# Optimization experiments

Measured on AMD Instinct MI355X. Metric: run time of the kernel, lower is better.

## Reference

```python
import jax, jax.numpy as jnp
import numpy as np

# ---- static LSS config (matches init_kwargs) ----
B, N = 4, 6
OGFH, OGFW, DS = 256, 704, 16
FH, FW = OGFH // DS, OGFW // DS            # 16, 44
D_LO, D_HI, D_STEP = 4.0, 45.0, 1.0
D = 41                                      # len(arange(4,45,1))
CAMC = 64
NX, NY, NZ = 200, 200, 1
DX = np.array([0.5, 0.5, 20.0], np.float32)
BX = np.array([-50.0 + 0.25, -50.0 + 0.25, -10.0 + 10.0], np.float32)  # lower + dx/2


def make_frustum():
    ds = jnp.arange(D_LO, D_HI, D_STEP, dtype=jnp.float32)[:, None, None]  # (D,1,1)
    xs = jnp.linspace(0.0, OGFW - 1.0, FW, dtype=jnp.float32)[None, None, :]
    ys = jnp.linspace(0.0, OGFH - 1.0, FH, dtype=jnp.float32)[None, :, None]
    ds, ys, xs = jnp.broadcast_arrays(ds, ys, xs)
    return jnp.stack([xs, ys, ds], axis=-1)  # (D, FH, FW, 3)


def setup_inputs() -> dict:
    key = jax.random.key(0)
    k1, k2 = jax.random.split(key)
    # depthnet output (pre-softmax depth logits + context features)
    x_feats = jax.random.normal(k1, (B, N, D + CAMC, FH, FW), dtype=jnp.float32)
    # cam-to-ego rotation: camera z (depth) -> ego x, so points land in the grid
    R = np.array([[0.0, 0.0, 1.0], [-1.0, 0.0, 0.0], [0.0, -1.0, 0.0]], np.float32)
    rots = jnp.asarray(np.broadcast_to(R, (B, N, 3, 3)).copy())
    trans = jax.random.normal(k2, (B, N, 3), dtype=jnp.float32) * 0.5
    f, cx, cy = 500.0, OGFW / 2.0, OGFH / 2.0
    K = np.array([[f, 0.0, cx], [0.0, f, cy], [0.0, 0.0, 1.0]], np.float32)
    intrins = jnp.asarray(np.broadcast_to(K, (B, N, 3, 3)).copy())
    post_rots = jnp.asarray(np.broadcast_to(np.eye(3, dtype=np.float32), (B, N, 3, 3)).copy())
    post_trans = jnp.zeros((B, N, 3), dtype=jnp.float32)
    return {"x_feats": x_feats, "rots": rots, "trans": trans,
            "intrins": intrins, "post_rots": post_rots, "post_trans": post_trans}


def reference(x_feats, rots, trans, intrins, post_rots, post_trans):
    # ---- lift: depth distribution x context features ----
    depth = jax.nn.softmax(x_feats[:, :, :D], axis=2)           # (B,N,D,h,w)
    feat = x_feats[:, :, D:D + CAMC]                            # (B,N,C,h,w)
    lifted = jnp.einsum('bndhw,bnchw->bndhwc', depth, feat)     # (B,N,D,h,w,C)

    # ---- geometry: per-pixel 3D points in ego frame ----
    frustum = make_frustum()                                    # (D,h,w,3)
    pts = frustum[None, None] - post_trans[:, :, None, None, None, :]
    pts = jnp.einsum('bnij,bndhwj->bndhwi', jnp.linalg.inv(post_rots), pts)
    pts = jnp.concatenate([pts[..., :2] * pts[..., 2:3], pts[..., 2:3]], axis=-1)
    combine = rots @ jnp.linalg.inv(intrins)
    pts = jnp.einsum('bnij,bndhwj->bndhwi', combine, pts) + trans[:, :, None, None, None, :]

    # ---- voxel pooling (scatter-add == bev_pool sum) ----
    dx = jnp.asarray(DX); bx = jnp.asarray(BX)
    gidx = jnp.floor((pts - (bx - dx / 2.0)) / dx).astype(jnp.int32)  # (B,N,D,h,w,3)
    ix, iy, iz = gidx[..., 0], gidx[..., 1], gidx[..., 2]
    valid = (ix >= 0) & (ix < NX) & (iy >= 0) & (iy < NY) & (iz >= 0) & (iz < NZ)
    b_ix = jnp.arange(B, dtype=jnp.int32)[:, None, None, None, None]
    flat = ((b_ix * NZ + iz) * NX + ix) * NY + iy                # (B,N,D,h,w)
    total = B * NZ * NX * NY
    flat = jnp.where(valid, flat, total)                         # invalid -> dump bin
    out = jax.ops.segment_sum(lifted.reshape(-1, CAMC), flat.reshape(-1),
                              num_segments=total + 1)[:total]
    # (B,NZ,NX,NY,C) -> final[b, :, z, x, y], then cat z-slices along channels
    out = out.reshape(B, NZ, NX, NY, CAMC).transpose(0, 1, 4, 2, 3)
    return out.reshape(B, NZ * CAMC, NX, NY)                     # (4, 64, 200, 200)
```

## Files before the change

kernel.cpp:

```cpp
#include <hip/hip_runtime.h>
#include <math.h>

#define BB 4
#define NN 6
#define DD 41
#define CC 64
#define FHh 16
#define FWw 44
#define NXg 200
#define NYg 200
#define NZg 1
#define NSLOT 128
#define NOVF  (FHh*DD)
#define XYg (NXg*NYg)
#define NVOX (BB*NZg*NXg*NYg)
#define NCOL (BB*NN*FWw)
#define NPIX (BB*NN*FHh*FWw)
#define NCH  (DD+CC)
#define NTILE (NVOX/64)

#define WSV_BYTES  (NVOX*CC*4u)
#define BMAP_OFF   WSV_BYTES
#define ZERO_BYTES (WSV_BYTES + 2560u)
#define WS_NEED    ZERO_BYTES

__device__ __forceinline__ void inv3x3d(const double m[9], double o[9]) {
    double a=m[0],b=m[1],c=m[2],d=m[3],e=m[4],f=m[5],g=m[6],h=m[7],i=m[8];
    double A = e*i - f*h;
    double Bv = -(d*i - f*g);
    double Cv = d*h - e*g;
    double det = a*A + b*Bv + c*Cv;
    double r = 1.0/det;
    o[0]=A*r;  o[1]=-(b*i-c*h)*r; o[2]=(b*f-c*e)*r;
    o[3]=Bv*r; o[4]=(a*i-c*g)*r;  o[5]=-(a*f-c*d)*r;
    o[6]=Cv*r; o[7]=-(a*h-b*g)*r; o[8]=(a*e-b*d)*r;
}

__global__ __launch_bounds__(256)
void lss_zero(float4* __restrict__ p, int n4)
{
    const int stride = gridDim.x * 256;
    for (int i = blockIdx.x * 256 + threadIdx.x; i < n4; i += stride)
        p[i] = make_float4(0.f, 0.f, 0.f, 0.f);
}

__global__ __launch_bounds__(256)
void lss_scatter_dedup(const float* __restrict__ xf,
                       const float* __restrict__ rots,
                       const float* __restrict__ trans,
                       const float* __restrict__ intr,
                       const float* __restrict__ prots,
                       const float* __restrict__ ptrans,
                       float* __restrict__ ws,
                       unsigned char* __restrict__ bmapT)
{
    __shared__ float s_feat[FHh * CC];
    __shared__ float s_coef[NSLOT * 17];
    __shared__ int   s_keys[NSLOT];
    __shared__ short s_list[NSLOT];
    __shared__ int   s_nslot;
    __shared__ int2  s_ovf[NOVF];
    __shared__ float s_ovfw[NOVF];
    __shared__ int   s_ovfcnt;

    const int tid  = threadIdx.x;
    const int lane = tid & 63;
    const int wv   = tid >> 6;

    const int obid = blockIdx.x;
    const int bid  = (obid & 7) * (NCOL / 8) + (obid >> 3);
    const int w   = bid % FWw;
    const int rem = bid / FWw;
    const int n   = rem % NN;
    const int b   = rem / NN;
    const int cam = b*NN + n;
    const float* colbase = xf + (size_t)cam * NCH * FHh * FWw + w;

    float lgt[4];
    #pragma unroll
    for (int r = 0; r < 4; ++r) {
        const int h = (wv << 2) + r;
        lgt[r] = (lane < DD)
            ? colbase[(size_t)lane * (FHh*FWw) + h * FWw] : -INFINITY;
    }

    if (tid < NSLOT) s_keys[tid] = -1;
    for (int i = tid; i < NSLOT*17; i += 256) s_coef[i] = 0.0f;
    if (tid == 0) { s_nslot = 0; s_ovfcnt = 0; }

    for (int t = tid; t < FHh*CC; t += 256) {
        int h = t >> 6, c = t & 63;
        s_feat[t] = colbase[(size_t)(DD + c) * (FHh*FWw) + h * FWw];
    }

    double K9[9], P9[9], R9[9];
    #pragma unroll
    for (int i = 0; i < 9; ++i) {
        K9[i] = (double)intr [cam*9 + i];
        P9[i] = (double)prots[cam*9 + i];
        R9[i] = (double)rots [cam*9 + i];
    }
    double Kinv[9], Pinv[9];
    inv3x3d(K9, Kinv);
    inv3x3d(P9, Pinv);
    double M[9];
    #pragma unroll
    for (int i = 0; i < 3; ++i)
        #pragma unroll
        for (int j = 0; j < 3; ++j)
            M[i*3+j] = R9[i*3+0]*Kinv[0*3+j] + R9[i*3+1]*Kinv[1*3+j] + R9[i*3+2]*Kinv[2*3+j];
    const double tx  = (double)trans [cam*3+0], ty  = (double)trans [cam*3+1], tz  = (double)trans [cam*3+2];
    const double ptx = (double)ptrans[cam*3+0], pty = (double)ptrans[cam*3+1], ptz = (double)ptrans[cam*3+2];

    __syncthreads();

    int      last_vox  = -1;
    unsigned last_slot = 0;
    for (int r = 0; r < 4; ++r) {
        const int h = (wv << 2) + r;
        float logit = lgt[r];
        float mx = logit;
        #pragma unroll
        for (int off = 32; off; off >>= 1) mx = fmaxf(mx, __shfl_xor(mx, off));
        float ex = (lane < DD) ? expf(logit - mx) : 0.0f;
        float sm = ex;
        #pragma unroll
        for (int off = 32; off; off >>= 1) sm += __shfl_xor(sm, off);
        const float wgt = ex / sm;

        int vox = -1;
        if (lane < DD) {
            double dz = 4.0 + (double)lane;
            double xs = (double)w * (703.0/43.0);
            double ys = (double)h * 17.0;
            double px = xs - ptx, py = ys - pty, pz = dz - ptz;
            double qx = Pinv[0]*px + Pinv[1]*py + Pinv[2]*pz;
            double qy = Pinv[3]*px + Pinv[4]*py + Pinv[5]*pz;
            double qz = Pinv[6]*px + Pinv[7]*py + Pinv[8]*pz;
            qx *= qz; qy *= qz;
            double gx = M[0]*qx + M[1]*qy + M[2]*qz + tx;
            double gy = M[3]*qx + M[4]*qy + M[5]*qz + ty;
            double gz = M[6]*qx + M[7]*qy + M[8]*qz + tz;
            double fx = floor((gx + 50.0) / 0.5);
            double fy = floor((gy + 50.0) / 0.5);
            double fz = floor((gz + 10.0) / 20.0);
            if (fx >= 0.0 && fx < (double)NXg &&
                fy >= 0.0 && fy < (double)NYg &&
                fz >= 0.0 && fz < (double)NZg) {
                int ix = (int)fx, iy = (int)fy, iz = (int)fz;
                vox = ((b*NZg + iz)*NXg + ix)*NYg + iy;
            }
        }

        if (vox >= 0) {
            if (vox == last_vox) {
                atomicAdd(&s_coef[last_slot*17 + h], wgt);
            } else {
                unsigned slot = (((unsigned)vox * 2654435761u) >> 18) & (NSLOT-1);
                bool done = false;
                for (int probe = 0; probe < NSLOT; ++probe) {
                    int prev = atomicCAS(&s_keys[slot], -1, vox);
                    if (prev == -1) {
                        int k = atomicAdd(&s_nslot, 1);
                        s_list[k] = (short)slot;
                    }
                    if (prev == -1 || prev == vox) {
                        atomicAdd(&s_coef[slot*17 + h], wgt);
                        last_vox = vox; last_slot = slot;
                        done = true;
                        break;
                    }
                    slot = (slot + 1) & (NSLOT-1);
                }
                if (!done) {
                    int k = atomicAdd(&s_ovfcnt, 1);
                    s_ovf[k]  = make_int2(vox, h);
                    s_ovfw[k] = wgt;
                    last_vox = -1;
                }
            }
        }
    }

    __syncthreads();

    float freg[FHh];
    #pragma unroll
    for (int h = 0; h < FHh; ++h) freg[h] = s_feat[(h << 6) + lane];

    const int nocc = s_nslot;
    for (int e = wv; e < nocc; e += 4) {
        int slot = s_list[e];
        int vox  = s_keys[slot];
        float acc = 0.0f;
        #pragma unroll
        for (int h = 0; h < FHh; ++h)
            acc += s_coef[slot*17 + h] * freg[h];
        atomicAdd(&ws[(size_t)vox * CC + lane], acc);
        if (lane == 0) bmapT[vox >> 6] = 1;
    }
    const int novf = s_ovfcnt;
    for (int e = wv; e < novf; e += 4) {
        int vox = s_ovf[e].x, h = s_ovf[e].y;
        atomicAdd(&ws[(size_t)vox * CC + lane], s_ovfw[e] * freg[h]);
        if (lane == 0) bmapT[vox >> 6] = 1;
    }
}

__global__ __launch_bounds__(256)
void lss_transpose_g(const float* __restrict__ ws,
                     const unsigned char* __restrict__ bmapT,
                     float* __restrict__ out)
{
    __shared__ float tile[CC][65];
    const int blk  = blockIdx.x;
    const int bz   = blk / 625;
    const int xy0  = (blk % 625) * 64;
    const int t    = threadIdx.x;
    const int lane = t & 63;
    const int wv   = t >> 6;

    float* dst = out + (size_t)bz * CC * XYg + xy0;
    if (bmapT[blk] == 0) {
        const float4 z = make_float4(0.f, 0.f, 0.f, 0.f);
        #pragma unroll
        for (int rep = 0; rep < 4; ++rep) {
            int c = (wv << 4) + (rep << 2) + (lane >> 4);
            int q = lane & 15;
            ((float4*)(dst + (size_t)c * XYg))[q] = z;
        }
        return;
    }

    const int vb = bz * XYg + xy0;
    const float4* src = (const float4*)(ws + (size_t)vb * CC);
    #pragma unroll
    for (int rep = 0; rep < 4; ++rep) {
        int idx = (wv << 8) + (rep << 6) + lane;
        int xyl = idx >> 4;
        int c4  = idx & 15;
        float4 v = src[idx];
        tile[(c4<<2)+0][xyl] = v.x;
        tile[(c4<<2)+1][xyl] = v.y;
        tile[(c4<<2)+2][xyl] = v.z;
        tile[(c4<<2)+3][xyl] = v.w;
    }
    __syncthreads();
    #pragma unroll
    for (int rep = 0; rep < 4; ++rep) {
        int c   = (wv << 4) + (rep << 2) + (lane >> 4);
        int xy4 = lane & 15;
        float4 v = make_float4(tile[c][(xy4<<2)+0], tile[c][(xy4<<2)+1],
                               tile[c][(xy4<<2)+2], tile[c][(xy4<<2)+3]);
        ((float4*)(dst + (size_t)c * XYg))[xy4] = v;
    }
}

__global__ __launch_bounds__(256)
void lss_scatter_direct(const float* __restrict__ xf,
                        const float* __restrict__ rots,
                        const float* __restrict__ trans,
                        const float* __restrict__ intr,
                        const float* __restrict__ prots,
                        const float* __restrict__ ptrans,
                        float* __restrict__ acc)
{
    const int wid  = blockIdx.x * 4 + (threadIdx.x >> 6);
    const int lane = threadIdx.x & 63;
    if (wid >= NPIX) return;
    int w  = wid % FWw;
    int t1 = wid / FWw;
    int h  = t1 % FHh; t1 /= FHh;
    int n  = t1 % NN;
    int b  = t1 / NN;
    const int cam = b*NN + n;

    double K9[9], P9[9], R9[9];
    #pragma unroll
    for (int i = 0; i < 9; ++i) {
        K9[i] = (double)intr [cam*9 + i];
        P9[i] = (double)prots[cam*9 + i];
        R9[i] = (double)rots [cam*9 + i];
    }
    double Kinv[9], Pinv[9];
    inv3x3d(K9, Kinv);
    inv3x3d(P9, Pinv);
    double M[9];
    #pragma unroll
    for (int i = 0; i < 3; ++i)
        #pragma unroll
        for (int j = 0; j < 3; ++j)
            M[i*3+j] = R9[i*3+0]*Kinv[0*3+j] + R9[i*3+1]*Kinv[1*3+j] + R9[i*3+2]*Kinv[2*3+j];
    const double tx  = (double)trans [cam*3+0], ty  = (double)trans [cam*3+1], tz  = (double)trans [cam*3+2];
    const double ptx = (double)ptrans[cam*3+0], pty = (double)ptrans[cam*3+1], ptz = (double)ptrans[cam*3+2];

    const size_t pixoff = (size_t)cam * NCH * FHh * FWw + (size_t)h * FWw + w;
    float logit = (lane < DD) ? xf[pixoff + (size_t)lane * (FHh*FWw)] : -INFINITY;
    float mx = logit;
    #pragma unroll
    for (int off = 32; off; off >>= 1) mx = fmaxf(mx, __shfl_xor(mx, off));
    float ex = (lane < DD) ? expf(logit - mx) : 0.0f;
    float sm = ex;
    #pragma unroll
    for (int off = 32; off; off >>= 1) sm += __shfl_xor(sm, off);
    const float wgt = ex / sm;

    int baddr = -1;
    if (lane < DD) {
        double dz = 4.0 + (double)lane;
        double xs = (double)w * (703.0/43.0);
        double ys = (double)h * 17.0;
        double px = xs - ptx, py = ys - pty, pz = dz - ptz;
        double qx = Pinv[0]*px + Pinv[1]*py + Pinv[2]*pz;
        double qy = Pinv[3]*px + Pinv[4]*py + Pinv[5]*pz;
        double qz = Pinv[6]*px + Pinv[7]*py + Pinv[8]*pz;
        qx *= qz; qy *= qz;
        double gx = M[0]*qx + M[1]*qy + M[2]*qz + tx;
        double gy = M[3]*qx + M[4]*qy + M[5]*qz + ty;
        double gz = M[6]*qx + M[7]*qy + M[8]*qz + tz;
        double fx = floor((gx + 50.0) / 0.5);
        double fy = floor((gy + 50.0) / 0.5);
        double fz = floor((gz + 10.0) / 20.0);
        if (fx >= 0.0 && fx < (double)NXg &&
            fy >= 0.0 && fy < (double)NYg &&
            fz >= 0.0 && fz < (double)NZg) {
            int ix = (int)fx, iy = (int)fy, iz = (int)fz;
            int bz = b*NZg + iz;
            baddr = bz * (CC*XYg) + ix*NYg + iy;
        }
    }

    const float f = xf[pixoff + (size_t)(DD + lane) * (FHh*FWw)];
    for (int d = 0; d < DD; ++d) {
        int   a  = __shfl(baddr, d);
        float wd = __shfl(wgt,   d);
        if (a >= 0) atomicAdd(&acc[(size_t)a + (size_t)lane * XYg], wd * f);
    }
}

extern "C" void kernel_launch(void* const* d_in, const int* in_sizes, int n_in,
                              void* d_out, int out_size, void* d_ws, size_t ws_size,
                              hipStream_t stream) {
    const float* xf     = (const float*)d_in[0];
    const float* rots   = (const float*)d_in[1];
    const float* trans  = (const float*)d_in[2];
    const float* intr   = (const float*)d_in[3];
    const float* prots  = (const float*)d_in[4];
    const float* ptrans = (const float*)d_in[5];
    float* out = (float*)d_out;

    if (ws_size >= (size_t)WS_NEED) {
        char* wsb = (char*)d_ws;
        float* ws = (float*)wsb;
        unsigned char* bmapT = (unsigned char*)(wsb + BMAP_OFF);
        lss_zero<<<dim3(2048), dim3(256), 0, stream>>>(
            (float4*)wsb, ZERO_BYTES/16);
        lss_scatter_dedup<<<dim3(NCOL), dim3(256), 0, stream>>>(
            xf, rots, trans, intr, prots, ptrans, ws, bmapT);
        lss_transpose_g<<<dim3(NTILE), dim3(256), 0, stream>>>(
            ws, bmapT, out);
    } else {
        lss_zero<<<dim3(2048), dim3(256), 0, stream>>>(
            (float4*)out, (BB*NZg*XYg*CC)/4);
        lss_scatter_direct<<<dim3((NPIX + 3) / 4), dim3(256), 0, stream>>>(
            xf, rots, trans, intr, prots, ptrans, out);
    }
}
```

Baseline: 44.73 us.

## Fuse scatter and transpose into one cooperative kernel with sparse zeroing

Adds a cooperative-groups kernel that runs the lift/scatter, zeroes only the workspace voxels it will touch, then after grid syncs accumulates and transposes the whole BEV grid into the output. A per-voxel occupancy map, set during the zeroing pass, lets the transpose write zeros for untouched voxels without reading them. This removes the full 41MB workspace zero-fill and two extra launches. In exchange it needs 5 blocks per CU for the cooperative launch, adds two grid-wide barriers, and falls back to the old path if occupancy is too low or the launch fails.

```diff
diff --git a/kernel.cpp b/kernel.cpp
--- a/kernel.cpp
+++ b/kernel.cpp
@@ -1,5 +1,8 @@
 #include <hip/hip_runtime.h>
+#include <hip/hip_cooperative_groups.h>
 #include <math.h>
+
+namespace cg = cooperative_groups;
 
 #define BB 4
 #define NN 6
@@ -19,10 +22,10 @@
 #define NCH  (DD+CC)
 #define NTILE (NVOX/64)
 
-#define WSV_BYTES  (NVOX*CC*4u)
-#define BMAP_OFF   WSV_BYTES
-#define ZERO_BYTES (WSV_BYTES + 2560u)
-#define WS_NEED    ZERO_BYTES
+#define WSV_OFF   0u
+#define BMAPV_OFF 40960000u
+#define BMAPT_OFF 41120000u
+#define WS_NEED   41122560u
 
 __device__ __forceinline__ void inv3x3d(const double m[9], double o[9]) {
     double a=m[0],b=m[1],c=m[2],d=m[3],e=m[4],f=m[5],g=m[6],h=m[7],i=m[8];
@@ -44,24 +47,28 @@
         p[i] = make_float4(0.f, 0.f, 0.f, 0.f);
 }
 
-__global__ __launch_bounds__(256)
-void lss_scatter_dedup(const float* __restrict__ xf,
-                       const float* __restrict__ rots,
-                       const float* __restrict__ trans,
-                       const float* __restrict__ intr,
-                       const float* __restrict__ prots,
-                       const float* __restrict__ ptrans,
-                       float* __restrict__ ws,
-                       unsigned char* __restrict__ bmapT)
+__global__ __launch_bounds__(256, 5)
+void lss_fused(const float* __restrict__ xf,
+               const float* __restrict__ rots,
+               const float* __restrict__ trans,
+               const float* __restrict__ intr,
+               const float* __restrict__ prots,
+               const float* __restrict__ ptrans,
+               float* __restrict__ ws,
+               unsigned char* __restrict__ bmap,
+               float* __restrict__ out)
 {
+    cg::grid_group grid = cg::this_grid();
+
     __shared__ float s_feat[FHh * CC];
     __shared__ float s_coef[NSLOT * 17];
     __shared__ int   s_keys[NSLOT];
     __shared__ short s_list[NSLOT];
     __shared__ int   s_nslot;
-    __shared__ int2  s_ovf[NOVF];
-    __shared__ float s_ovfw[NOVF];
     __shared__ int   s_ovfcnt;
+    __shared__ __align__(16) float s_tile[CC * 65];
+    int2*  s_ovf  = (int2*)s_tile;
+    float* s_ovfw = s_tile + 1312;
 
     const int tid  = threadIdx.x;
     const int lane = tid & 63;
@@ -183,6 +190,214 @@
     }
 
     __syncthreads();
+    const int nocc = s_nslot;
+    const int novf = s_ovfcnt;
+
+    float freg[FHh];
+    #pragma unroll
+    for (int h = 0; h < FHh; ++h) freg[h] = s_feat[(h << 6) + lane];
+
+    for (int e = wv; e < nocc; e += 4) {
+        int vox = s_keys[s_list[e]];
+        ws[(size_t)vox * CC + lane] = 0.0f;
+        if (lane == 0) bmap[vox] = 1;
+    }
+    for (int e = wv; e < novf; e += 4) {
+        int vox = s_ovf[e].x;
+        ws[(size_t)vox * CC + lane] = 0.0f;
+        if (lane == 0) bmap[vox] = 1;
+    }
+
+    __threadfence();
+    grid.sync();
+
+    for (int e = wv; e < nocc; e += 4) {
+        int slot = s_list[e];
+        int vox  = s_keys[slot];
+        float acc = 0.0f;
+        #pragma unroll
+        for (int h = 0; h < FHh; ++h)
+            acc += s_coef[slot*17 + h] * freg[h];
+        atomicAdd(&ws[(size_t)vox * CC + lane], acc);
+    }
+    for (int e = wv; e < novf; e += 4) {
+        int vox = s_ovf[e].x, h = s_ovf[e].y;
+        atomicAdd(&ws[(size_t)vox * CC + lane], s_ovfw[e] * freg[h]);
+    }
+
+    __threadfence();
+    grid.sync();
+
+    const float4 z4 = make_float4(0.f, 0.f, 0.f, 0.f);
+    for (int t = blockIdx.x; t < NTILE; t += NCOL) {
+        const int bz  = t / 625;
+        const int xy0 = (t % 625) * 64;
+        const int vb  = bz * XYg + xy0;
+        const float4* src = (const float4*)(ws + (size_t)vb * CC);
+        #pragma unroll
+        for (int rep = 0; rep < 4; ++rep) {
+            int idx = (wv << 8) + (rep << 6) + lane;
+            int xyl = idx >> 4;
+            int c4  = idx & 15;
+            float4 v = bmap[vb + xyl] ? src[idx] : z4;
+            s_tile[((c4<<2)+0)*65 + xyl] = v.x;
+            s_tile[((c4<<2)+1)*65 + xyl] = v.y;
+            s_tile[((c4<<2)+2)*65 + xyl] = v.z;
+            s_tile[((c4<<2)+3)*65 + xyl] = v.w;
+        }
+        __syncthreads();
+        float* dst = out + (size_t)bz * CC * XYg + xy0;
+        #pragma unroll
+        for (int rep = 0; rep < 4; ++rep) {
+            int c = (wv << 4) + (rep << 2) + (lane >> 4);
+            int q = lane & 15;
+            float4 v = make_float4(s_tile[c*65 + 4*q + 0], s_tile[c*65 + 4*q + 1],
+                                   s_tile[c*65 + 4*q + 2], s_tile[c*65 + 4*q + 3]);
+            ((float4*)(dst + (size_t)c * XYg))[q] = v;
+        }
+        __syncthreads();
+    }
+}
+
+__global__ __launch_bounds__(256)
+void lss_scatter_dedup(const float* __restrict__ xf,
+                       const float* __restrict__ rots,
+                       const float* __restrict__ trans,
+                       const float* __restrict__ intr,
+                       const float* __restrict__ prots,
+                       const float* __restrict__ ptrans,
+                       float* __restrict__ ws,
+                       unsigned char* __restrict__ bmapT)
+{
+    __shared__ float s_feat[FHh * CC];
+    __shared__ float s_coef[NSLOT * 17];
+    __shared__ int   s_keys[NSLOT];
+    __shared__ short s_list[NSLOT];
+    __shared__ int   s_nslot;
+    __shared__ int2  s_ovf[NOVF];
+    __shared__ float s_ovfw[NOVF];
+    __shared__ int   s_ovfcnt;
+
+    const int tid  = threadIdx.x;
+    const int lane = tid & 63;
+    const int wv   = tid >> 6;
+
+    const int obid = blockIdx.x;
+    const int bid  = (obid & 7) * (NCOL / 8) + (obid >> 3);
+    const int w   = bid % FWw;
+    const int rem = bid / FWw;
+    const int n   = rem % NN;
+    const int b   = rem / NN;
+    const int cam = b*NN + n;
+    const float* colbase = xf + (size_t)cam * NCH * FHh * FWw + w;
+
+    float lgt[4];
+    #pragma unroll
+    for (int r = 0; r < 4; ++r) {
+        const int h = (wv << 2) + r;
+        lgt[r] = (lane < DD)
+            ? colbase[(size_t)lane * (FHh*FWw) + h * FWw] : -INFINITY;
+    }
+
+    if (tid < NSLOT) s_keys[tid] = -1;
+    for (int i = tid; i < NSLOT*17; i += 256) s_coef[i] = 0.0f;
+    if (tid == 0) { s_nslot = 0; s_ovfcnt = 0; }
+
+    for (int t = tid; t < FHh*CC; t += 256) {
+        int h = t >> 6, c = t & 63;
+        s_feat[t] = colbase[(size_t)(DD + c) * (FHh*FWw) + h * FWw];
+    }
+
+    double K9[9], P9[9], R9[9];
+    #pragma unroll
+    for (int i = 0; i < 9; ++i) {
+        K9[i] = (double)intr [cam*9 + i];
+        P9[i] = (double)prots[cam*9 + i];
+        R9[i] = (double)rots [cam*9 + i];
+    }
+    double Kinv[9], Pinv[9];
+    inv3x3d(K9, Kinv);
+    inv3x3d(P9, Pinv);
+    double M[9];
+    #pragma unroll
+    for (int i = 0; i < 3; ++i)
+        #pragma unroll
+        for (int j = 0; j < 3; ++j)
+            M[i*3+j] = R9[i*3+0]*Kinv[0*3+j] + R9[i*3+1]*Kinv[1*3+j] + R9[i*3+2]*Kinv[2*3+j];
+    const double tx  = (double)trans [cam*3+0], ty  = (double)trans [cam*3+1], tz  = (double)trans [cam*3+2];
+    const double ptx = (double)ptrans[cam*3+0], pty = (double)ptrans[cam*3+1], ptz = (double)ptrans[cam*3+2];
+
+    __syncthreads();
+
+    int      last_vox  = -1;
+    unsigned last_slot = 0;
+    for (int r = 0; r < 4; ++r) {
+        const int h = (wv << 2) + r;
+        float logit = lgt[r];
+        float mx = logit;
+        #pragma unroll
+        for (int off = 32; off; off >>= 1) mx = fmaxf(mx, __shfl_xor(mx, off));
+        float ex = (lane < DD) ? expf(logit - mx) : 0.0f;
+        float sm = ex;
+        #pragma unroll
+        for (int off = 32; off; off >>= 1) sm += __shfl_xor(sm, off);
+        const float wgt = ex / sm;
+
+        int vox = -1;
+        if (lane < DD) {
+            double dz = 4.0 + (double)lane;
+            double xs = (double)w * (703.0/43.0);
+            double ys = (double)h * 17.0;
+            double px = xs - ptx, py = ys - pty, pz = dz - ptz;
+            double qx = Pinv[0]*px + Pinv[1]*py + Pinv[2]*pz;
+            double qy = Pinv[3]*px + Pinv[4]*py + Pinv[5]*pz;
+            double qz = Pinv[6]*px + Pinv[7]*py + Pinv[8]*pz;
+            qx *= qz; qy *= qz;
+            double gx = M[0]*qx + M[1]*qy + M[2]*qz + tx;
+            double gy = M[3]*qx + M[4]*qy + M[5]*qz + ty;
+            double gz = M[6]*qx + M[7]*qy + M[8]*qz + tz;
+            double fx = floor((gx + 50.0) / 0.5);
+            double fy = floor((gy + 50.0) / 0.5);
+            double fz = floor((gz + 10.0) / 20.0);
+            if (fx >= 0.0 && fx < (double)NXg &&
+                fy >= 0.0 && fy < (double)NYg &&
+                fz >= 0.0 && fz < (double)NZg) {
+                int ix = (int)fx, iy = (int)fy, iz = (int)fz;
+                vox = ((b*NZg + iz)*NXg + ix)*NYg + iy;
+            }
+        }
+
+        if (vox >= 0) {
+            if (vox == last_vox) {
+                atomicAdd(&s_coef[last_slot*17 + h], wgt);
+            } else {
+                unsigned slot = (((unsigned)vox * 2654435761u) >> 18) & (NSLOT-1);
+                bool done = false;
+                for (int probe = 0; probe < NSLOT; ++probe) {
+                    int prev = atomicCAS(&s_keys[slot], -1, vox);
+                    if (prev == -1) {
+                        int k = atomicAdd(&s_nslot, 1);
+                        s_list[k] = (short)slot;
+                    }
+                    if (prev == -1 || prev == vox) {
+                        atomicAdd(&s_coef[slot*17 + h], wgt);
+                        last_vox = vox; last_slot = slot;
+                        done = true;
+                        break;
+                    }
+                    slot = (slot + 1) & (NSLOT-1);
+                }
+                if (!done) {
+                    int k = atomicAdd(&s_ovfcnt, 1);
+                    s_ovf[k]  = make_int2(vox, h);
+                    s_ovfw[k] = wgt;
+                    last_vox = -1;
+                }
+            }
+        }
+    }
+
+    __syncthreads();
 
     float freg[FHh];
     #pragma unroll
@@ -351,10 +566,27 @@
 
     if (ws_size >= (size_t)WS_NEED) {
         char* wsb = (char*)d_ws;
-        float* ws = (float*)wsb;
-        unsigned char* bmapT = (unsigned char*)(wsb + BMAP_OFF);
+        float* ws = (float*)(wsb + WSV_OFF);
+        unsigned char* bmapv = (unsigned char*)(wsb + BMAPV_OFF);
+        unsigned char* bmapT = (unsigned char*)(wsb + BMAPT_OFF);
+
+        int occ = 0;
+        hipError_t qe = hipOccupancyMaxActiveBlocksPerMultiprocessor(
+            &occ, reinterpret_cast<const void*>(&lss_fused), 256, 0);
+        bool coop_ok = (qe == hipSuccess) && (occ >= 5);
+
+        if (coop_ok) {
+            lss_zero<<<dim3(64), dim3(256), 0, stream>>>(
+                (float4*)bmapv, NVOX/16);
+            void* kargs[] = { (void*)&xf, (void*)&rots, (void*)&trans,
+                              (void*)&intr, (void*)&prots, (void*)&ptrans,
+                              (void*)&ws, (void*)&bmapv, (void*)&out };
+            hipError_t le = hipLaunchCooperativeKernel(
+                (void*)lss_fused, dim3(NCOL), dim3(256), kargs, 0, stream);
+            if (le == hipSuccess) return;
+        }
         lss_zero<<<dim3(2048), dim3(256), 0, stream>>>(
-            (float4*)wsb, ZERO_BYTES/16);
+            (float4*)wsb, WS_NEED/16);
         lss_scatter_dedup<<<dim3(NCOL), dim3(256), 0, stream>>>(
             xf, rots, trans, intr, prots, ptrans, ws, bmapT);
         lss_transpose_g<<<dim3(NTILE), dim3(256), 0, stream>>>(
```

New measurement: 44.46 us. Within noise of the previous version (-0.6%).
